# Kernel tuning notes

Hardware: AMD Instinct MI355X
Metric: run time of the kernel (lower is better)

The kernel has to match this reference:

```python
import jax, jax.numpy as jnp
import numpy as np
from jax import lax

EPS = 1e-5

def _conv(x, w, b, stride):
    y = lax.conv_general_dilated(x, w, window_strides=(stride, stride), padding='VALID',
                                 dimension_numbers=('NCHW', 'OIHW', 'NCHW'))
    return y + b[None, :, None, None]

def _upsample_zero(x, s):
    B, C, H, W = x.shape
    z = jnp.zeros((B, C, H * s, W * s), dtype=x.dtype)
    return z.at[:, :, ::s, ::s].set(x)

def setup_inputs() -> dict:
    key = jax.random.key(0)
    ks = jax.random.split(key, 12)
    B, C, H, W = 512, 3, 128, 128
    FLAT = 3 * 65 * 65  # 12675 per the shape chain
    sc = lambda fan_in: 1.0 / np.sqrt(fan_in)
    return {
        'x': jax.random.normal(ks[0], (B, C, H, W), dtype=jnp.float32),
        'bn_gamma': jnp.ones((C,), jnp.float32),
        'bn_beta': jnp.zeros((C,), jnp.float32),
        'w1': jax.random.normal(ks[1], (3, 3, 5, 5), jnp.float32) * sc(3 * 25),
        'b1': jax.random.normal(ks[2], (3,), jnp.float32) * 0.01,
        'w2': jax.random.normal(ks[3], (3, 3, 5, 5), jnp.float32) * sc(3 * 25),
        'b2': jax.random.normal(ks[4], (3,), jnp.float32) * 0.01,
        'fc1_w': jax.random.normal(ks[5], (128, FLAT), jnp.float32) * sc(FLAT),
        'fc1_b': jnp.zeros((128,), jnp.float32),
        'fc2_w': jax.random.normal(ks[6], (10, 128), jnp.float32) * sc(128),
        'fc2_b': jnpp if False else jnp.zeros((10,), jnp.float32),
    }

def reference(x, bn_gamma, bn_beta, w1, b1, w2, b2, fc1_w, fc1_b, fc2_w, fc2_b):
    # BatchNorm1d over active sites (= all original pixels; zero-pad sites are inactive)
    mean = x.mean(axis=(0, 2, 3))
    var = ((x - mean[None, :, None, None]) ** 2).mean(axis=(0, 2, 3))  # biased, as torch BN
    xn = (x - mean[None, :, None, None]) * lax.rsqrt(var + EPS)[None, :, None, None]
    xn = xn * bn_gamma[None, :, None, None] + bn_beta[None, :, None, None]
    # SparseZeroPad2d(1) -> [B,3,130,130]
    h = jnp.pad(xn, ((0, 0), (0, 0), (1, 1), (1, 1)))
    # cv1 (k5,s5) -> [B,3,26,26]; SparseScale2d(5) -> zeros interleaved [B,3,130,130]
    h = _upsample_zero(_conv(h, w1, b1, 5), 5)
    h = jax.nn.relu(h)
    # cv2 (k5,s5) -> [B,3,26,26]; scale -> [B,3,130,130]
    h = _upsample_zero(_conv(h, w2, b2, 5), 5)
    h = jax.nn.relu(h)
    # SparseMaxPool2d(2,2) -> [B,3,65,65]; features >= 0 so dense pool matches sparse pool
    h = lax.reduce_window(h, -jnp.inf, lax.max, (1, 1, 2, 2), (1, 1, 2, 2), 'VALID')
    # flatten -> dropout(eval=identity) -> fc1 -> relu -> fc2 -> log_softmax
    f = h.reshape(h.shape[0], -1)
    f = jax.nn.relu(f @ fc1_w.T + fc1_b)
    logits = f @ fc2_w.T + fc2_b
    return jax.nn.log_softmax(logits, axis=1)
```

## Files before the change

kernel.cpp:

```cpp
#include <hip/hip_runtime.h>

#define BN_EPS 1e-5f

typedef short short8 __attribute__((ext_vector_type(8)));
typedef float f32x4 __attribute__((ext_vector_type(4)));
typedef unsigned short ushort;

__device__ inline ushort f2bf(float f) {
  unsigned int u = __float_as_uint(f);
  u += 0x7FFFu + ((u >> 16) & 1u);
  return (ushort)(u >> 16);
}


#define NPOS 346112
#define LROW 144

__global__ __launch_bounds__(256) void k_convraw(
    const float* __restrict__ x,
    const float* __restrict__ w1g,
    float* __restrict__ S,
    float* __restrict__ psumS)
{
  __shared__ float s_xp[65 * LROW];
  __shared__ float red[4][2];
  const int tid = threadIdx.x;
  const int bid = blockIdx.x;
  const int h = bid & 1;
  const int c = (bid >> 1) % 3;
  const int b = bid / 6;

  const int zrow = h ? 64 : 0;
  for (int i = tid; i < LROW; i += 256) s_xp[zrow * LROW + i] = 0.f;
  if (tid < 65) { s_xp[tid * LROW + 3] = 0.f; s_xp[tid * LROW + 132] = 0.f; }

  const int r0 = h ? 64 : 0;
  const int off0 = h ? 0 : 1;

  const float4* xp = (const float4*)(x + ((size_t)b * 3 + c) * 16384 + (size_t)r0 * 128);
  float s = 0.f, q = 0.f;
  #pragma unroll
  for (int i = 0; i < 8; i++) {
    int v = i * 256 + tid;
    float4 a4 = xp[v];
    int lr = (v >> 5) + off0;
    int col = (v & 31) << 2;
    float* d = &s_xp[lr * LROW + col + 4];
    d[0] = a4.x; d[1] = a4.y; d[2] = a4.z; d[3] = a4.w;
    s += (a4.x + a4.y) + (a4.z + a4.w);
    q += (a4.x * a4.x + a4.y * a4.y) + (a4.z * a4.z + a4.w * a4.w);
  }
  __syncthreads();

  const float* wc = w1g + c * 25;
  #pragma unroll
  for (int pp = 0; pp < 2; pp++) {
    int p = tid + pp * 256;
    if (p < 338) {
      int ol = p / 26, ox = p - ol * 26;
      const float* base = &s_xp[(5 * ol) * LROW + 5 * ox + 3];
      float a0 = 0.f, a1 = 0.f, a2 = 0.f;
      #pragma unroll
      for (int ky = 0; ky < 5; ky++) {
        #pragma unroll
        for (int kx = 0; kx < 5; kx++) {
          float v = base[ky * LROW + kx];
          a0 += wc[ky * 5 + kx] * v;
          a1 += wc[75 + ky * 5 + kx] * v;
          a2 += wc[150 + ky * 5 + kx] * v;
        }
      }
      int oy = h * 13 + ol;
      size_t gp = (size_t)b * 676 + oy * 26 + ox;
      S[(size_t)(c * 3 + 0) * NPOS + gp] = a0;
      S[(size_t)(c * 3 + 1) * NPOS + gp] = a1;
      S[(size_t)(c * 3 + 2) * NPOS + gp] = a2;
    }
  }

  #pragma unroll
  for (int off = 32; off; off >>= 1) {
    s += __shfl_down(s, off);
    q += __shfl_down(q, off);
  }
  int lane = tid & 63, wv = tid >> 6;
  if (lane == 0) { red[wv][0] = s; red[wv][1] = q; }
  __syncthreads();
  if (tid == 0)
    psumS[c * 1024 + b * 2 + h] = (red[0][0] + red[1][0]) + (red[2][0] + red[3][0]);
  if (tid == 1)
    psumS[(3 + c) * 1024 + b * 2 + h] = (red[0][1] + red[1][1]) + (red[2][1] + red[3][1]);
}

__global__ __launch_bounds__(384) void k_reduce(const float* __restrict__ psumS,
                                                float* __restrict__ stats) {
  int w = threadIdx.x >> 6, lane = threadIdx.x & 63;
  const float* src = psumS + w * 1024;
  float acc = 0.f;
  #pragma unroll
  for (int k = 0; k < 16; k++) acc += src[lane + 64 * k];
  #pragma unroll
  for (int off = 32; off; off >>= 1) acc += __shfl_down(acc, off);
  if (lane == 0) stats[w] = acc;
}

__device__ inline float gval(const float* __restrict__ row, int k) {
  if (k >= 2028) return 0.f;
  int c = k / 676;
  int rem = k - c * 676;
  int oy = rem / 26, ox = rem - oy * 26;
  int col = c * 4225 + ((5 * oy) >> 1) * 65 + ((5 * ox) >> 1);
  return row[col];
}

__global__ __launch_bounds__(256) void k_gather(const float* __restrict__ fc1_w,
                                                ushort* __restrict__ WgtB) {
  int gid = blockIdx.x * 256 + threadIdx.x;
  int l = gid & 63;
  int n = ((gid >> 12) << 4) + (l & 15);
  int kbase = (((gid >> 6) & 63) << 5) + ((l >> 4) << 3);
  const float* row = fc1_w + n * 12675;
  uint4 o;
  unsigned int w[4];
  #pragma unroll
  for (int i = 0; i < 4; i++) {
    ushort lo = f2bf(gval(row, kbase + 2 * i));
    ushort hi = f2bf(gval(row, kbase + 2 * i + 1));
    w[i] = (unsigned int)lo | ((unsigned int)hi << 16);
  }
  o.x = w[0]; o.y = w[1]; o.z = w[2]; o.w = w[3];
  ((uint4*)WgtB)[gid] = o;
}

__global__ __launch_bounds__(256) void k_combine(
    const float* __restrict__ S,
    const float* __restrict__ stats,
    const float* __restrict__ gamma, const float* __restrict__ beta,
    const float* __restrict__ w1, const float* __restrict__ b1,
    const float* __restrict__ w2, const float* __restrict__ b2,
    ushort* __restrict__ featB)
{
  __shared__ float s_w1[225];
  __shared__ float s_w2[9];
  __shared__ float s_scale[3], s_shift[3], s_b1[3], s_b2[3];
  __shared__ float s_T[9][9];
  const int tid = threadIdx.x;
  if (tid < 225) s_w1[tid] = w1[tid];
  if (tid < 9) s_w2[tid] = w2[tid * 25];
  if (tid < 3) {
    const float N = 512.f * 128.f * 128.f;
    float mean = stats[tid] / N;
    float var = stats[3 + tid] / N - mean * mean;
    float sc = gamma[tid] * rsqrtf(var + BN_EPS);
    s_scale[tid] = sc;
    s_shift[tid] = beta[tid] - mean * sc;
    s_b1[tid] = b1[tid];
    s_b2[tid] = b2[tid];
  }
  __syncthreads();
  if (tid < 81) {
    int cls = tid / 9, oc = tid - (tid / 9) * 9;
    int rcl = cls / 3, ccl = cls - rcl * 3;
    int o = oc / 3, c = oc - o * 3;
    int ky0 = (rcl == 0) ? 1 : 0, ky1 = (rcl == 2) ? 3 : 4;
    int kx0 = (ccl == 0) ? 1 : 0, kx1 = (ccl == 2) ? 3 : 4;
    float t = 0.f;
    for (int ky = ky0; ky <= ky1; ky++)
      for (int kx = kx0; kx <= kx1; kx++)
        t += s_w1[o * 75 + c * 25 + ky * 5 + kx];
    s_T[cls][oc] = t;
  }
  __syncthreads();

  int gpos = blockIdx.x * 256 + tid;
  int b = gpos / 676;
  int pos = gpos - b * 676;
  int oy = pos / 26, ox = pos - oy * 26;
  int rcl = (oy == 0) ? 0 : ((oy == 25) ? 2 : 1);
  int ccl = (ox == 0) ? 0 : ((ox == 25) ? 2 : 1);
  int cls = rcl * 3 + ccl;

  float h[3];
  #pragma unroll
  for (int o = 0; o < 3; o++) {
    float a = s_b1[o];
    #pragma unroll
    for (int c = 0; c < 3; c++) {
      a += s_scale[c] * S[(size_t)(c * 3 + o) * NPOS + gpos];
      a += s_shift[c] * s_T[cls][o * 3 + c];
    }
    h[o] = fmaxf(a, 0.f);
  }
  ushort* fb = featB + (size_t)b * 2048;
  #pragma unroll
  for (int o = 0; o < 3; o++) {
    float v = s_b2[o] + s_w2[3 * o] * h[0] + s_w2[3 * o + 1] * h[1] + s_w2[3 * o + 2] * h[2];
    fb[o * 676 + pos] = f2bf(fmaxf(v, 0.f));
  }
  if (pos < 20) fb[2028 + pos] = 0;
}

__global__ __launch_bounds__(512) void k_fc(
    const ushort* __restrict__ featB,
    const ushort* __restrict__ WgtB,
    const float* __restrict__ fc1_b,
    const float* __restrict__ fc2_w, const float* __restrict__ fc2_b,
    float* __restrict__ out)
{
  __shared__ float s_f[16][132];
  __shared__ float s_lg[16][10];
  const int tid = threadIdx.x;
  const int lane = tid & 63;
  const int t = tid >> 6;
  const int m0 = blockIdx.x * 16;

  const ushort* aptr = featB + (size_t)(m0 + (lane & 15)) * 2048 + ((lane >> 4) << 3);
  const ushort* bptr = WgtB + ((size_t)t * 4096 + lane) * 8;

  f32x4 acc = {0.f, 0.f, 0.f, 0.f};
  #pragma unroll 4
  for (int kk = 0; kk < 64; kk++) {
    short8 a = *(const short8*)(aptr + kk * 32);
    short8 bfr = *(const short8*)(bptr + kk * 512);
    acc = __builtin_amdgcn_mfma_f32_16x16x32_bf16(a, bfr, acc, 0, 0, 0);
  }
  {
    int n = t * 16 + (lane & 15);
    float bias = fc1_b[n];
    int mb = (lane >> 4) << 2;
    #pragma unroll
    for (int r = 0; r < 4; r++)
      s_f[mb + r][n] = fmaxf(acc[r] + bias, 0.f);
  }
  __syncthreads();

  if (tid < 160) {
    int m = tid & 15, q = tid >> 4;
    const float* wr = fc2_w + q * 128;
    float a2 = fc2_b[q];
    #pragma unroll 8
    for (int k = 0; k < 128; k++) a2 += wr[k] * s_f[m][k];
    s_lg[m][q] = a2;
  }
  __syncthreads();

  if (tid < 16) {
    float mx = s_lg[tid][0];
    #pragma unroll
    for (int q = 1; q < 10; q++) mx = fmaxf(mx, s_lg[tid][q]);
    float se = 0.f;
    #pragma unroll
    for (int q = 0; q < 10; q++) se += expf(s_lg[tid][q] - mx);
    float lse = mx + logf(se);
    float* op = out + (size_t)(m0 + tid) * 10;
    #pragma unroll
    for (int q = 0; q < 10; q++) op[q] = s_lg[tid][q] - lse;
  }
}

extern "C" void kernel_launch(void* const* d_in, const int* in_sizes, int n_in,
                              void* d_out, int out_size, void* d_ws, size_t ws_size,
                              hipStream_t stream) {
  const float* x      = (const float*)d_in[0];
  const float* gamma  = (const float*)d_in[1];
  const float* beta   = (const float*)d_in[2];
  const float* w1     = (const float*)d_in[3];
  const float* b1     = (const float*)d_in[4];
  const float* w2     = (const float*)d_in[5];
  const float* b2     = (const float*)d_in[6];
  const float* fc1_w  = (const float*)d_in[7];
  const float* fc1_b  = (const float*)d_in[8];
  const float* fc2_w  = (const float*)d_in[9];
  const float* fc2_b  = (const float*)d_in[10];
  float* out = (float*)d_out;
  float* wsf = (float*)d_ws;

  float* stats  = wsf;
  float* psumS  = wsf + 64;
  ushort* WgtB  = (ushort*)(wsf + 16384);
  ushort* featB = (ushort*)(wsf + 262144);
  float* S      = wsf + 786432;

  k_convraw<<<3072, 256, 0, stream>>>(x, w1, S, psumS);
  k_gather<<<128, 256, 0, stream>>>(fc1_w, WgtB);
  k_reduce<<<1, 384, 0, stream>>>(psumS, stats);
  k_combine<<<1352, 256, 0, stream>>>(S, stats, gamma, beta, w1, b1, w2, b2, featB);
  k_fc<<<32, 512, 0, stream>>>(featB, WgtB, fc1_b, fc2_w, fc2_b, out);
}
```

Before: 56.80 us.

## Split first conv into 10-row strips per block for finer-grained parallelism

Each conv block used to load half an image channel (about 65 padded rows) into shared memory. It now loads a 10-row strip, producing two output rows, so the grid grows from 3072 to 19968 blocks and shared memory per block drops sharply. Each of three wavefronts now computes one output channel instead of every thread computing all three. BN partial sums are written per block and reduced by a wider 6-block reduce kernel. The aim is higher occupancy and better latency hiding on the bandwidth-bound input read, at the cost of more block launches, idle lanes, and a larger partial-sum reduction.

```diff
diff --git a/kernel.cpp b/kernel.cpp
--- a/kernel.cpp
+++ b/kernel.cpp
@@ -15,67 +15,60 @@
 
 #define NPOS 346112
 #define LROW 144
-
-__global__ __launch_bounds__(256) void k_convraw(
+#define NBLK 19968
+
+__global__ __launch_bounds__(256, 8) void k_convraw(
     const float* __restrict__ x,
     const float* __restrict__ w1g,
     float* __restrict__ S,
     float* __restrict__ psumS)
 {
-  __shared__ float s_xp[65 * LROW];
+  __shared__ float s_xp[10 * LROW];
   __shared__ float red[4][2];
   const int tid = threadIdx.x;
   const int bid = blockIdx.x;
-  const int h = bid & 1;
-  const int c = (bid >> 1) % 3;
-  const int b = bid / 6;
-
-  const int zrow = h ? 64 : 0;
-  for (int i = tid; i < LROW; i += 256) s_xp[zrow * LROW + i] = 0.f;
-  if (tid < 65) { s_xp[tid * LROW + 3] = 0.f; s_xp[tid * LROW + 132] = 0.f; }
-
-  const int r0 = h ? 64 : 0;
-  const int off0 = h ? 0 : 1;
-
-  const float4* xp = (const float4*)(x + ((size_t)b * 3 + c) * 16384 + (size_t)r0 * 128);
+  const int k = bid % 13;
+  const int c = (bid / 13) % 3;
+  const int b = bid / 39;
+
+  if (tid < 10) {
+    s_xp[tid * LROW + 3] = 0.f;
+    s_xp[tid * LROW + 132] = 0.f;
+  }
+
+  const float* xc = x + ((size_t)b * 3 + c) * 16384;
   float s = 0.f, q = 0.f;
   #pragma unroll
-  for (int i = 0; i < 8; i++) {
-    int v = i * 256 + tid;
-    float4 a4 = xp[v];
-    int lr = (v >> 5) + off0;
-    int col = (v & 31) << 2;
-    float* d = &s_xp[lr * LROW + col + 4];
-    d[0] = a4.x; d[1] = a4.y; d[2] = a4.z; d[3] = a4.w;
-    s += (a4.x + a4.y) + (a4.z + a4.w);
-    q += (a4.x * a4.x + a4.y * a4.y) + (a4.z * a4.z + a4.w * a4.w);
-  }
-  __syncthreads();
-
-  const float* wc = w1g + c * 25;
-  #pragma unroll
-  for (int pp = 0; pp < 2; pp++) {
-    int p = tid + pp * 256;
-    if (p < 338) {
-      int ol = p / 26, ox = p - ol * 26;
-      const float* base = &s_xp[(5 * ol) * LROW + 5 * ox + 3];
-      float a0 = 0.f, a1 = 0.f, a2 = 0.f;
+  for (int u = 0; u < 2; u++) {
+    int v = tid + u * 256;
+    if (v < 320) {
+      int j = v >> 5, col4 = (v & 31) << 2;
+      int r = 10 * k - 1 + j;
+      float4 a4 = {0.f, 0.f, 0.f, 0.f};
+      if (r >= 0 && r < 128) a4 = *(const float4*)(xc + r * 128 + col4);
+      float* d = &s_xp[j * LROW + col4 + 4];
+      d[0] = a4.x; d[1] = a4.y; d[2] = a4.z; d[3] = a4.w;
+      s += (a4.x + a4.y) + (a4.z + a4.w);
+      q += (a4.x * a4.x + a4.y * a4.y) + (a4.z * a4.z + a4.w * a4.w);
+    }
+  }
+  __syncthreads();
+
+  const int w = tid >> 6, lane = tid & 63;
+  if (w < 3 && lane < 52) {
+    int ol = lane >= 26 ? 1 : 0;
+    int ox = lane - ol * 26;
+    const float* wk = w1g + w * 75 + c * 25;
+    const float* base = &s_xp[(5 * ol) * LROW + 5 * ox + 3];
+    float a = 0.f;
+    #pragma unroll
+    for (int ky = 0; ky < 5; ky++) {
       #pragma unroll
-      for (int ky = 0; ky < 5; ky++) {
-        #pragma unroll
-        for (int kx = 0; kx < 5; kx++) {
-          float v = base[ky * LROW + kx];
-          a0 += wc[ky * 5 + kx] * v;
-          a1 += wc[75 + ky * 5 + kx] * v;
-          a2 += wc[150 + ky * 5 + kx] * v;
-        }
-      }
-      int oy = h * 13 + ol;
-      size_t gp = (size_t)b * 676 + oy * 26 + ox;
-      S[(size_t)(c * 3 + 0) * NPOS + gp] = a0;
-      S[(size_t)(c * 3 + 1) * NPOS + gp] = a1;
-      S[(size_t)(c * 3 + 2) * NPOS + gp] = a2;
+      for (int kx = 0; kx < 5; kx++)
+        a += wk[ky * 5 + kx] * base[ky * LROW + kx];
     }
+    int oy = 2 * k + ol;
+    S[(size_t)(c * 3 + w) * NPOS + (size_t)b * 676 + oy * 26 + ox] = a;
   }
 
   #pragma unroll
@@ -83,25 +76,31 @@
     s += __shfl_down(s, off);
     q += __shfl_down(q, off);
   }
-  int lane = tid & 63, wv = tid >> 6;
-  if (lane == 0) { red[wv][0] = s; red[wv][1] = q; }
+  if (lane == 0) { red[w][0] = s; red[w][1] = q; }
   __syncthreads();
   if (tid == 0)
-    psumS[c * 1024 + b * 2 + h] = (red[0][0] + red[1][0]) + (red[2][0] + red[3][0]);
+    psumS[(size_t)c * NBLK + bid] = (red[0][0] + red[1][0]) + (red[2][0] + red[3][0]);
   if (tid == 1)
-    psumS[(3 + c) * 1024 + b * 2 + h] = (red[0][1] + red[1][1]) + (red[2][1] + red[3][1]);
-}
-
-__global__ __launch_bounds__(384) void k_reduce(const float* __restrict__ psumS,
-                                                float* __restrict__ stats) {
-  int w = threadIdx.x >> 6, lane = threadIdx.x & 63;
-  const float* src = psumS + w * 1024;
+    psumS[(size_t)(3 + c) * NBLK + bid] = (red[0][1] + red[1][1]) + (red[2][1] + red[3][1]);
+}
+
+__global__ __launch_bounds__(1024) void k_reduce(const float* __restrict__ psumS,
+                                                 float* __restrict__ stats) {
+  const int sidx = blockIdx.x;
+  const float* src = psumS + (size_t)sidx * NBLK;
   float acc = 0.f;
-  #pragma unroll
-  for (int k = 0; k < 16; k++) acc += src[lane + 64 * k];
+  for (int i = threadIdx.x; i < NBLK; i += 1024) acc += src[i];
   #pragma unroll
   for (int off = 32; off; off >>= 1) acc += __shfl_down(acc, off);
-  if (lane == 0) stats[w] = acc;
+  __shared__ float r[16];
+  if ((threadIdx.x & 63) == 0) r[threadIdx.x >> 6] = acc;
+  __syncthreads();
+  if (threadIdx.x == 0) {
+    float t = 0.f;
+    #pragma unroll
+    for (int i = 0; i < 16; i++) t += r[i];
+    stats[sidx] = t;
+  }
 }
 
 __device__ inline float gval(const float* __restrict__ row, int k) {
@@ -239,7 +238,7 @@
     const float* wr = fc2_w + q * 128;
     float a2 = fc2_b[q];
     #pragma unroll 8
-    for (int k = 0; k < 128; k++) a2 += wr[k] * s_f[m][k];
+    for (int n = 0; n < 128; n++) a2 += wr[n] * s_f[m][n];
     s_lg[m][q] = a2;
   }
   __syncthreads();
@@ -277,13 +276,13 @@
 
   float* stats  = wsf;
   float* psumS  = wsf + 64;
-  ushort* WgtB  = (ushort*)(wsf + 16384);
+  ushort* WgtB  = (ushort*)(wsf + 131072);
   ushort* featB = (ushort*)(wsf + 262144);
   float* S      = wsf + 786432;
 
-  k_convraw<<<3072, 256, 0, stream>>>(x, w1, S, psumS);
+  k_convraw<<<NBLK, 256, 0, stream>>>(x, w1, S, psumS);
   k_gather<<<128, 256, 0, stream>>>(fc1_w, WgtB);
-  k_reduce<<<1, 384, 0, stream>>>(psumS, stats);
+  k_reduce<<<6, 1024, 0, stream>>>(psumS, stats);
   k_combine<<<1352, 256, 0, stream>>>(S, stats, gamma, beta, w1, b1, w2, b2, featB);
   k_fc<<<32, 512, 0, stream>>>(featB, WgtB, fc1_b, fc2_w, fc2_b, out);
 }
```

Measured after the change: 71.20 us. +25.3%, slower.
